# Performance work log

Measured on AMD Instinct MI355X. Metric: run time of the kernel, lower is better.

The kernel has to match this reference:

```python
import jax, jax.numpy as jnp
import numpy as np

N_NODES = 100000
N_EDGES = 1600000
DIMS = [128, 128, 128, 64]  # in, h1, h2, out


def setup_inputs() -> dict:
    key = jax.random.key(0)
    ks = jax.random.split(key, 12)
    inp = {
        "x": jax.random.normal(ks[0], (N_NODES, DIMS[0]), dtype=jnp.float32),
        "edge_index": jax.random.randint(ks[1], (2, N_EDGES), 0, N_NODES, dtype=jnp.int64),
        "edge_weights": jax.random.uniform(ks[2], (N_EDGES,), dtype=jnp.float32),
    }
    for i in range(3):
        inp[f"W{i+1}"] = jax.random.normal(ks[3 + 2 * i], (DIMS[i], DIMS[i + 1]), dtype=jnp.float32) * 0.05
        inp[f"b{i+1}"] = jax.random.normal(ks[4 + 2 * i], (DIMS[i + 1],), dtype=jnp.float32) * 0.01
    return inp


def gcn_conv(x, src, dst, w, W, b, n_nodes):
    # PyG GCNConv: linear transform, symmetric gcn_norm with self-loops (weight 1), scatter-add, bias.
    xw = x @ W                                            # [N, out]
    deg = jax.ops.segment_sum(w, dst, num_segments=n_nodes) + 1.0  # self-loop weight 1
    dinv = jnp.where(deg > 0, jax.lax.rsqrt(deg), 0.0)    # deg^{-1/2}
    norm = dinv[src] * w * dinv[dst]                      # [E]
    out = jax.ops.segment_sum(norm[:, None] * xw[src], dst, num_segments=n_nodes)
    out = out + (dinv * dinv)[:, None] * xw               # self-loop message
    return out + b


def reference(x, edge_index, edge_weights, W1, b1, W2, b2, W3, b3):
    src, dst = edge_index[0], edge_index[1]
    n = x.shape[0]
    # layer 1: GCNConv -> dropout(p=0) -> relu
    h = jax.nn.relu(gcn_conv(x, src, dst, edge_weights, W1, b1, n))
    # layer 2
    h = jax.nn.relu(gcn_conv(h, src, dst, edge_weights, W2, b2, n))
    # layer 3: activation 'none' -> Identity
    h = gcn_conv(h, src, dst, edge_weights, W3, b3, n)
    return h
```

## Files before the change

kernel.cpp:

```cpp
#include <hip/hip_runtime.h>
#include <hip/hip_fp16.h>
#include <math.h>


typedef __bf16 bf16x8 __attribute__((ext_vector_type(8)));
typedef float f32x4 __attribute__((ext_vector_type(4)));

union BF8 {
  unsigned short u[8];
  uint4 q;
  bf16x8 v;
};

__device__ __forceinline__ unsigned short rne_bf16(float f) {
  unsigned u = __float_as_uint(f);
  u += 0x7fff + ((u >> 16) & 1);
  return (unsigned short)(u >> 16);
}
__device__ __forceinline__ float bf16_to_f(unsigned short h) {
  return __uint_as_float((unsigned)h << 16);
}

__global__ __launch_bounds__(256) void prep_w1_kernel(const float* __restrict__ W,
    unsigned short* __restrict__ WTg) {
  const int t = threadIdx.x;
#pragma unroll
  for (int it = 0; it < 8; ++it) {
    int n = t % 128;
    int kc = it * 2 + t / 128;
    int k0 = kc * 8;
    BF8 hh, ll;
#pragma unroll
    for (int j = 0; j < 8; ++j) {
      float w = W[(size_t)(k0 + j) * 128 + n];
      unsigned short hb = rne_bf16(w);
      hh.u[j] = hb;
      ll.u[j] = rne_bf16(w - bf16_to_f(hb));
    }
    int kk = k0 ^ ((n & 7) << 3);
    *(uint4*)&WTg[(size_t)n * 128 + kk] = hh.q;
    *(uint4*)&WTg[16384 + (size_t)n * 128 + kk] = ll.q;
  }
}

__device__ __forceinline__ void gemm_body_g(const float* __restrict__ A,
    const unsigned short* __restrict__ WTg, unsigned short* __restrict__ Ch,
    int M, int bid) {
  constexpr int NF = 8;
  const int t = threadIdx.x;
  const int wv = t >> 6;
  const int l = t & 63;
  const int lr = l & 15;
  const int lg = l >> 4;
  const int arow_i = bid * 64 + wv * 16 + lr;
  const bool rv = arow_i < M;
  const float* arow = A + (size_t)arow_i * 128;

  f32x4 acc[NF] = {};
  float4 p0 = make_float4(0.f, 0.f, 0.f, 0.f), p1 = p0;
  if (rv) {
    p0 = *(const float4*)&arow[lg * 8];
    p1 = *(const float4*)&arow[lg * 8 + 4];
  }
#pragma unroll 1
  for (int ks = 0; ks < 4; ++ks) {
    int nkb = ((ks < 3) ? (ks + 1) * 32 : ks * 32) + lg * 8;
    float4 q0 = make_float4(0.f, 0.f, 0.f, 0.f), q1 = q0;
    if (rv) {
      q0 = *(const float4*)&arow[nkb];
      q1 = *(const float4*)&arow[nkb + 4];
    }
    float av[8] = {p0.x, p0.y, p0.z, p0.w, p1.x, p1.y, p1.z, p1.w};
    BF8 ah, al;
#pragma unroll
    for (int j = 0; j < 8; ++j) {
      unsigned short hb = rne_bf16(av[j]);
      ah.u[j] = hb;
      al.u[j] = rne_bf16(av[j] - bf16_to_f(hb));
    }
    int kidx = ks * 32 + lg * 8;
#pragma unroll
    for (int nf = 0; nf < NF; ++nf) {
      int n = nf * 16 + lr;
      int kk = kidx ^ ((n & 7) << 3);
      BF8 bh, bl;
      bh.q = *(const uint4*)&WTg[(size_t)n * 128 + kk];
      bl.q = *(const uint4*)&WTg[16384 + (size_t)n * 128 + kk];
      acc[nf] = __builtin_amdgcn_mfma_f32_16x16x32_bf16(ah.v, bh.v, acc[nf], 0, 0, 0);
      acc[nf] = __builtin_amdgcn_mfma_f32_16x16x32_bf16(al.v, bh.v, acc[nf], 0, 0, 0);
      acc[nf] = __builtin_amdgcn_mfma_f32_16x16x32_bf16(ah.v, bl.v, acc[nf], 0, 0, 0);
    }
    p0 = q0; p1 = q1;
  }
  const int orow0 = bid * 64 + wv * 16 + lg * 4;
#pragma unroll
  for (int j = 0; j < 4; ++j) {
    int orow = orow0 + j;
    if (orow < M) {
      unsigned short* hr = Ch + (size_t)orow * 128;
#pragma unroll
      for (int nf = 0; nf < NF; ++nf)
        hr[nf * 16 + lr] = __half_as_ushort(__float2half(acc[nf][j]));
    }
  }
}

__global__ __launch_bounds__(256) void pre_gemm_fused_kernel(
    const float* __restrict__ x, const unsigned short* __restrict__ WT1g,
    unsigned short* __restrict__ Ch, int M,
    const int* __restrict__ ei, const float* __restrict__ ew,
    unsigned long long* __restrict__ packed, int* __restrict__ rank,
    int E, int edgeBlocks) {
  if ((int)blockIdx.x < edgeBlocks) {
    int e = blockIdx.x * 256 + threadIdx.x;
    if (e >= E) return;
    int d = ei[E + e];
    unsigned wfix = (unsigned)__float2uint_rn(ew[e] * 16777216.0f);
    unsigned long long inc = (1ULL << 32) | (unsigned long long)wfix;
    unsigned long long old = atomicAdd(&packed[d], inc);
    rank[e] = (int)(old >> 32);
  } else {
    gemm_body_g(x, WT1g, Ch, M, blockIdx.x - edgeBlocks);
  }
}

template <int NCOL>
__global__ __launch_bounds__(256) void gemm_mfma_kernel(
    const unsigned short* __restrict__ Ah, const float* __restrict__ W,
    unsigned short* __restrict__ Ch, int M) {
  constexpr int NF = NCOL / 16;
  __shared__ __align__(16) unsigned short WT[2][NCOL][128];
  const int t = threadIdx.x;
  constexpr int KC_PER_IT = 256 / NCOL;
#pragma unroll
  for (int it = 0; it < 16 / KC_PER_IT; ++it) {
    int n = t % NCOL;
    int kc = it * KC_PER_IT + t / NCOL;
    int k0 = kc * 8;
    BF8 hh, ll;
#pragma unroll
    for (int j = 0; j < 8; ++j) {
      float w = W[(size_t)(k0 + j) * NCOL + n];
      unsigned short hb = rne_bf16(w);
      hh.u[j] = hb;
      ll.u[j] = rne_bf16(w - bf16_to_f(hb));
    }
    int kk = k0 ^ ((n & 7) << 3);
    *(uint4*)&WT[0][n][kk] = hh.q;
    *(uint4*)&WT[1][n][kk] = ll.q;
  }
  __syncthreads();

  const int wv = t >> 6;
  const int l = t & 63;
  const int lr = l & 15;
  const int lg = l >> 4;
  const int arow_i = blockIdx.x * 64 + wv * 16 + lr;
  const bool rv = arow_i < M;
  const unsigned short* arowh = Ah + (size_t)arow_i * 128;

  f32x4 acc[NF] = {};
  uint4 ph = make_uint4(0, 0, 0, 0);
  if (rv) ph = *(const uint4*)&arowh[lg * 8];
#pragma unroll 1
  for (int ks = 0; ks < 4; ++ks) {
    int nkb = ((ks < 3) ? (ks + 1) * 32 : ks * 32) + lg * 8;
    uint4 qh = make_uint4(0, 0, 0, 0);
    if (rv) qh = *(const uint4*)&arowh[nkb];
    float av[8];
    {
      union { uint4 q; __half2 h2[4]; } uu;
      uu.q = ph;
#pragma unroll
      for (int j = 0; j < 4; ++j) {
        float2 f = __half22float2(uu.h2[j]);
        av[j * 2] = f.x; av[j * 2 + 1] = f.y;
      }
    }
    BF8 ah, al;
#pragma unroll
    for (int j = 0; j < 8; ++j) {
      unsigned short hb = rne_bf16(av[j]);
      ah.u[j] = hb;
      al.u[j] = rne_bf16(av[j] - bf16_to_f(hb));
    }
    int kidx = ks * 32 + lg * 8;
    BF8 bh[NF], bl[NF];
#pragma unroll
    for (int nf = 0; nf < NF; ++nf) {
      int n = nf * 16 + lr;
      int kk = kidx ^ ((n & 7) << 3);
      bh[nf].q = *(const uint4*)&WT[0][n][kk];
      bl[nf].q = *(const uint4*)&WT[1][n][kk];
    }
#pragma unroll
    for (int nf = 0; nf < NF; ++nf) {
      acc[nf] = __builtin_amdgcn_mfma_f32_16x16x32_bf16(ah.v, bh[nf].v, acc[nf], 0, 0, 0);
      acc[nf] = __builtin_amdgcn_mfma_f32_16x16x32_bf16(al.v, bh[nf].v, acc[nf], 0, 0, 0);
      acc[nf] = __builtin_amdgcn_mfma_f32_16x16x32_bf16(ah.v, bl[nf].v, acc[nf], 0, 0, 0);
    }
    ph = qh;
  }
  const int orow0 = blockIdx.x * 64 + wv * 16 + lg * 4;
#pragma unroll
  for (int j = 0; j < 4; ++j) {
    int orow = orow0 + j;
    if (orow < M) {
      unsigned short* hr = Ch + (size_t)orow * NCOL;
#pragma unroll
      for (int nf = 0; nf < NF; ++nf)
        hr[nf * 16 + lr] = __half_as_ushort(__float2half(acc[nf][j]));
    }
  }
}

__global__ __launch_bounds__(256) void dinv_kernel(const unsigned long long* __restrict__ packed,
    float* __restrict__ dinv, int n) {
  int i = blockIdx.x * 256 + threadIdx.x;
  if (i >= n) return;
  float deg = 1.0f + (float)(unsigned)(packed[i] & 0xffffffffULL) * (1.0f / 16777216.0f);
  dinv[i] = 1.0f / sqrtf(deg);
}

__global__ __launch_bounds__(1024) void scanA(const unsigned long long* __restrict__ packed,
    int* __restrict__ row_ptr, int* __restrict__ partials, int n) {
  __shared__ int sd[1024];
  int t = threadIdx.x;
  int i = blockIdx.x * 1024 + t;
  int v = (i < n) ? (int)(packed[i] >> 32) : 0;
  sd[t] = v;
  __syncthreads();
  for (int off = 1; off < 1024; off <<= 1) {
    int u = (t >= off) ? sd[t - off] : 0;
    __syncthreads();
    sd[t] += u;
    __syncthreads();
  }
  int incl = sd[t];
  if (i < n) row_ptr[i] = incl - v;
  if (t == 1023) partials[blockIdx.x] = incl;
}

__global__ __launch_bounds__(128) void scanB(int* partials, int nb) {
  __shared__ int sd[128];
  int t = threadIdx.x;
  int v = (t < nb) ? partials[t] : 0;
  sd[t] = v;
  __syncthreads();
  for (int off = 1; off < 128; off <<= 1) {
    int u = (t >= off) ? sd[t - off] : 0;
    __syncthreads();
    sd[t] += u;
    __syncthreads();
  }
  int incl = sd[t];
  partials[t] = incl - v;
  if (t == nb - 1) partials[255] = incl;
}

__global__ __launch_bounds__(1024) void scanC(int* row_ptr, const int* __restrict__ partials, int n) {
  int i = blockIdx.x * 1024 + threadIdx.x;
  if (i < n) row_ptr[i] += partials[blockIdx.x];
  if (i == 0) row_ptr[n] = partials[255];
}

__global__ __launch_bounds__(256) void fill_kernel(const int* __restrict__ ei,
    const float* __restrict__ ew, const float* __restrict__ dinv,
    const int* __restrict__ row_ptr, const int* __restrict__ rank,
    int2* __restrict__ epair, int E) {
  int e = blockIdx.x * 256 + threadIdx.x;
  if (e >= E) return;
  int s = ei[e], d = ei[E + e];
  float nw = dinv[s] * ew[e] * dinv[d];
  int p = row_ptr[d] + rank[e];
  epair[p] = make_int2(s, __float_as_int(nw));
}

template <int F, bool RELU, bool OUTF16>
__global__ __launch_bounds__(256) void agg_kernel(const unsigned short* __restrict__ xwh,
    const int* __restrict__ row_ptr, const int2* __restrict__ epair,
    const float* __restrict__ dinv, const float* __restrict__ bias,
    void* __restrict__ out, int Nn) {
  constexpr int LPN = F / 4;
  int t = blockIdx.x * 256 + threadIdx.x;
  int node = t / LPN;
  int lane = t % LPN;
  if (node >= Nn) return;
  const uint2* xh = (const uint2*)xwh;
  int start = row_ptr[node];
  int end = row_ptr[node + 1];
  float a0x = 0.f, a0y = 0.f, a0z = 0.f, a0w = 0.f;
  float a1x = 0.f, a1y = 0.f, a1z = 0.f, a1w = 0.f;
  int p = start;
  for (; p + 4 <= end; p += 4) {
    int2 e0 = epair[p];
    int2 e1 = epair[p + 1];
    int2 e2 = epair[p + 2];
    int2 e3 = epair[p + 3];
    uint2 u0 = xh[(size_t)e0.x * LPN + lane];
    uint2 u1 = xh[(size_t)e1.x * LPN + lane];
    uint2 u2 = xh[(size_t)e2.x * LPN + lane];
    uint2 u3 = xh[(size_t)e3.x * LPN + lane];
    float n0 = __int_as_float(e0.y), n1 = __int_as_float(e1.y);
    float n2 = __int_as_float(e2.y), n3 = __int_as_float(e3.y);
    float2 f0a = __half22float2(*(__half2*)&u0.x), f0b = __half22float2(*(__half2*)&u0.y);
    float2 f1a = __half22float2(*(__half2*)&u1.x), f1b = __half22float2(*(__half2*)&u1.y);
    float2 f2a = __half22float2(*(__half2*)&u2.x), f2b = __half22float2(*(__half2*)&u2.y);
    float2 f3a = __half22float2(*(__half2*)&u3.x), f3b = __half22float2(*(__half2*)&u3.y);
    a0x = fmaf(n0, f0a.x, a0x); a0y = fmaf(n0, f0a.y, a0y);
    a0z = fmaf(n0, f0b.x, a0z); a0w = fmaf(n0, f0b.y, a0w);
    a1x = fmaf(n1, f1a.x, a1x); a1y = fmaf(n1, f1a.y, a1y);
    a1z = fmaf(n1, f1b.x, a1z); a1w = fmaf(n1, f1b.y, a1w);
    a0x = fmaf(n2, f2a.x, a0x); a0y = fmaf(n2, f2a.y, a0y);
    a0z = fmaf(n2, f2b.x, a0z); a0w = fmaf(n2, f2b.y, a0w);
    a1x = fmaf(n3, f3a.x, a1x); a1y = fmaf(n3, f3a.y, a1y);
    a1z = fmaf(n3, f3b.x, a1z); a1w = fmaf(n3, f3b.y, a1w);
  }
  for (; p < end; ++p) {
    int2 pr = epair[p];
    float nw = __int_as_float(pr.y);
    uint2 u = xh[(size_t)pr.x * LPN + lane];
    float2 fa = __half22float2(*(__half2*)&u.x), fb = __half22float2(*(__half2*)&u.y);
    a0x = fmaf(nw, fa.x, a0x); a0y = fmaf(nw, fa.y, a0y);
    a0z = fmaf(nw, fb.x, a0z); a0w = fmaf(nw, fb.y, a0w);
  }
  float di = dinv[node];
  float sw = di * di;
  uint2 su = xh[(size_t)node * LPN + lane];
  float2 sa = __half22float2(*(__half2*)&su.x), sb = __half22float2(*(__half2*)&su.y);
  a0x = fmaf(sw, sa.x, a0x); a0y = fmaf(sw, sa.y, a0y);
  a0z = fmaf(sw, sb.x, a0z); a0w = fmaf(sw, sb.y, a0w);
  float4 b = ((const float4*)bias)[lane];
  float ox = a0x + a1x + b.x;
  float oy = a0y + a1y + b.y;
  float oz = a0z + a1z + b.z;
  float ow = a0w + a1w + b.w;
  if (RELU) {
    ox = fmaxf(ox, 0.f); oy = fmaxf(oy, 0.f);
    oz = fmaxf(oz, 0.f); ow = fmaxf(ow, 0.f);
  }
  if constexpr (OUTF16) {
    uint2 o;
    __half2 h0 = __float22half2_rn(make_float2(ox, oy));
    __half2 h1 = __float22half2_rn(make_float2(oz, ow));
    o.x = *reinterpret_cast<unsigned*>(&h0);
    o.y = *reinterpret_cast<unsigned*>(&h1);
    ((uint2*)out)[(size_t)node * LPN + lane] = o;
  } else {
    ((float4*)out)[(size_t)node * LPN + lane] = make_float4(ox, oy, oz, ow);
  }
}

extern "C" void kernel_launch(void* const* d_in, const int* in_sizes, int n_in,
                              void* d_out, int out_size, void* d_ws, size_t ws_size,
                              hipStream_t stream) {
  const float* x  = (const float*)d_in[0];
  const int*   ei = (const int*)d_in[1];
  const float* ew = (const float*)d_in[2];
  const float* W1 = (const float*)d_in[3];
  const float* b1 = (const float*)d_in[4];
  const float* W2 = (const float*)d_in[5];
  const float* b2 = (const float*)d_in[6];
  const float* W3 = (const float*)d_in[7];
  const float* b3 = (const float*)d_in[8];

  const int N = in_sizes[0] / 128;
  const int E = in_sizes[2];

  char* ws = (char*)d_ws;
  size_t off = 0;
  auto carve = [&](size_t bytes) -> void* {
    void* p = ws + off;
    off += (bytes + 255) & ~(size_t)255;
    return p;
  };
  unsigned long long* packed = (unsigned long long*)carve((size_t)N * 8);
  int*   rank    = (int*)carve((size_t)E * 4);
  float* dinv    = (float*)carve((size_t)N * 4);
  int*   row_ptr = (int*)carve((size_t)(N + 1) * 4);
  int*   parts   = (int*)carve(256 * 4);
  int2*  epair   = (int2*)carve((size_t)E * 8);
  unsigned short* bufH = (unsigned short*)carve((size_t)N * 128 * 2);
  unsigned short* bufI = (unsigned short*)carve((size_t)N * 128 * 2);
  unsigned short* WT1g = (unsigned short*)carve(2 * 128 * 128 * 2);
  (void)ws_size; (void)n_in; (void)out_size;

  const int nThreads = 256;
  int gN  = (N + nThreads - 1) / nThreads;
  int gE  = (E + nThreads - 1) / nThreads;
  int nb  = (N + 1023) / 1024;
  const int gMM = (N + 63) / 64;
  int gAgg128 = (N * 32 + nThreads - 1) / nThreads;
  int gAgg64  = (N * 16 + nThreads - 1) / nThreads;

  hipMemsetAsync(packed, 0, (size_t)N * 8, stream);
  prep_w1_kernel<<<1, nThreads, 0, stream>>>(W1, WT1g);

  pre_gemm_fused_kernel<<<gE + gMM, nThreads, 0, stream>>>(
      x, WT1g, bufH, N, ei, ew, packed, rank, E, gE);

  dinv_kernel<<<gN, nThreads, 0, stream>>>(packed, dinv, N);
  scanA<<<nb, 1024, 0, stream>>>(packed, row_ptr, parts, N);
  scanB<<<1, 128, 0, stream>>>(parts, nb);
  scanC<<<nb, 1024, 0, stream>>>(row_ptr, parts, N);
  fill_kernel<<<gE, nThreads, 0, stream>>>(ei, ew, dinv, row_ptr, rank, epair, E);

  agg_kernel<128, true, true><<<gAgg128, nThreads, 0, stream>>>(bufH, row_ptr, epair, dinv, b1, bufI, N);

  gemm_mfma_kernel<128><<<gMM, nThreads, 0, stream>>>(bufI, W2, bufH, N);
  agg_kernel<128, true, true><<<gAgg128, nThreads, 0, stream>>>(bufH, row_ptr, epair, dinv, b2, bufI, N);

  gemm_mfma_kernel<64><<<gMM, nThreads, 0, stream>>>(bufI, W3, bufH, N);
  agg_kernel<64, false, false><<<gAgg64, nThreads, 0, stream>>>(bufH, row_ptr, epair, dinv, b3, d_out, N);
}
```

Baseline: 366.1 us.

## Split layer-1 GEMM into 64-column slices with per-block LDS weight staging

Removes the separate W1 prep kernel. Each GEMM block now converts a 64-column slice of W1 into hi/lo bf16 in shared memory and reads B fragments from LDS instead of global memory, with twice as many blocks each computing half the columns. Fragment loads are also batched ahead of the MFMA chain. The cost is that every block redoes the W1 split and reads its A rows twice across the column halves, and the shared-memory allocation may lower occupancy for the fused edge-atomic blocks.

```diff
diff --git a/kernel.cpp b/kernel.cpp
--- a/kernel.cpp
+++ b/kernel.cpp
@@ -21,33 +21,31 @@
   return __uint_as_float((unsigned)h << 16);
 }
 
-__global__ __launch_bounds__(256) void prep_w1_kernel(const float* __restrict__ W,
-    unsigned short* __restrict__ WTg) {
+__device__ __forceinline__ void gemm_body_slice(const float* __restrict__ A,
+    const float* __restrict__ W, int ldw, int col0,
+    unsigned short* __restrict__ Ch, int ldc, int M, int bid) {
+  constexpr int NF = 4;
+  __shared__ __align__(16) unsigned short WT[2][64][128];
   const int t = threadIdx.x;
 #pragma unroll
-  for (int it = 0; it < 8; ++it) {
-    int n = t % 128;
-    int kc = it * 2 + t / 128;
+  for (int it = 0; it < 4; ++it) {
+    int n = t & 63;
+    int kc = it * 4 + (t >> 6);
     int k0 = kc * 8;
     BF8 hh, ll;
 #pragma unroll
     for (int j = 0; j < 8; ++j) {
-      float w = W[(size_t)(k0 + j) * 128 + n];
+      float w = W[(size_t)(k0 + j) * ldw + col0 + n];
       unsigned short hb = rne_bf16(w);
       hh.u[j] = hb;
       ll.u[j] = rne_bf16(w - bf16_to_f(hb));
     }
     int kk = k0 ^ ((n & 7) << 3);
-    *(uint4*)&WTg[(size_t)n * 128 + kk] = hh.q;
-    *(uint4*)&WTg[16384 + (size_t)n * 128 + kk] = ll.q;
-  }
-}
-
-__device__ __forceinline__ void gemm_body_g(const float* __restrict__ A,
-    const unsigned short* __restrict__ WTg, unsigned short* __restrict__ Ch,
-    int M, int bid) {
-  constexpr int NF = 8;
-  const int t = threadIdx.x;
+    *(uint4*)&WT[0][n][kk] = hh.q;
+    *(uint4*)&WT[1][n][kk] = ll.q;
+  }
+  __syncthreads();
+
   const int wv = t >> 6;
   const int l = t & 63;
   const int lr = l & 15;
@@ -79,16 +77,19 @@
       al.u[j] = rne_bf16(av[j] - bf16_to_f(hb));
     }
     int kidx = ks * 32 + lg * 8;
+    BF8 bh[NF], bl[NF];
 #pragma unroll
     for (int nf = 0; nf < NF; ++nf) {
       int n = nf * 16 + lr;
       int kk = kidx ^ ((n & 7) << 3);
-      BF8 bh, bl;
-      bh.q = *(const uint4*)&WTg[(size_t)n * 128 + kk];
-      bl.q = *(const uint4*)&WTg[16384 + (size_t)n * 128 + kk];
-      acc[nf] = __builtin_amdgcn_mfma_f32_16x16x32_bf16(ah.v, bh.v, acc[nf], 0, 0, 0);
-      acc[nf] = __builtin_amdgcn_mfma_f32_16x16x32_bf16(al.v, bh.v, acc[nf], 0, 0, 0);
-      acc[nf] = __builtin_amdgcn_mfma_f32_16x16x32_bf16(ah.v, bl.v, acc[nf], 0, 0, 0);
+      bh[nf].q = *(const uint4*)&WT[0][n][kk];
+      bl[nf].q = *(const uint4*)&WT[1][n][kk];
+    }
+#pragma unroll
+    for (int nf = 0; nf < NF; ++nf) {
+      acc[nf] = __builtin_amdgcn_mfma_f32_16x16x32_bf16(ah.v, bh[nf].v, acc[nf], 0, 0, 0);
+      acc[nf] = __builtin_amdgcn_mfma_f32_16x16x32_bf16(al.v, bh[nf].v, acc[nf], 0, 0, 0);
+      acc[nf] = __builtin_amdgcn_mfma_f32_16x16x32_bf16(ah.v, bl[nf].v, acc[nf], 0, 0, 0);
     }
     p0 = q0; p1 = q1;
   }
@@ -97,7 +98,7 @@
   for (int j = 0; j < 4; ++j) {
     int orow = orow0 + j;
     if (orow < M) {
-      unsigned short* hr = Ch + (size_t)orow * 128;
+      unsigned short* hr = Ch + (size_t)orow * ldc + col0;
 #pragma unroll
       for (int nf = 0; nf < NF; ++nf)
         hr[nf * 16 + lr] = __half_as_ushort(__float2half(acc[nf][j]));
@@ -106,7 +107,7 @@
 }
 
 __global__ __launch_bounds__(256) void pre_gemm_fused_kernel(
-    const float* __restrict__ x, const unsigned short* __restrict__ WT1g,
+    const float* __restrict__ x, const float* __restrict__ W1,
     unsigned short* __restrict__ Ch, int M,
     const int* __restrict__ ei, const float* __restrict__ ew,
     unsigned long long* __restrict__ packed, int* __restrict__ rank,
@@ -120,7 +121,8 @@
     unsigned long long old = atomicAdd(&packed[d], inc);
     rank[e] = (int)(old >> 32);
   } else {
-    gemm_body_g(x, WT1g, Ch, M, blockIdx.x - edgeBlocks);
+    int g = blockIdx.x - edgeBlocks;
+    gemm_body_slice(x, W1, 128, (g & 1) * 64, Ch, 128, M, g >> 1);
   }
 }
 
@@ -382,7 +384,6 @@
   int2*  epair   = (int2*)carve((size_t)E * 8);
   unsigned short* bufH = (unsigned short*)carve((size_t)N * 128 * 2);
   unsigned short* bufI = (unsigned short*)carve((size_t)N * 128 * 2);
-  unsigned short* WT1g = (unsigned short*)carve(2 * 128 * 128 * 2);
   (void)ws_size; (void)n_in; (void)out_size;
 
   const int nThreads = 256;
@@ -394,10 +395,8 @@
   int gAgg64  = (N * 16 + nThreads - 1) / nThreads;
 
   hipMemsetAsync(packed, 0, (size_t)N * 8, stream);
-  prep_w1_kernel<<<1, nThreads, 0, stream>>>(W1, WT1g);
-
-  pre_gemm_fused_kernel<<<gE + gMM, nThreads, 0, stream>>>(
-      x, WT1g, bufH, N, ei, ew, packed, rank, E, gE);
+  pre_gemm_fused_kernel<<<gE + 2 * gMM, nThreads, 0, stream>>>(
+      x, W1, bufH, N, ei, ew, packed, rank, E, gE);
 
   dinv_kernel<<<gN, nThreads, 0, stream>>>(packed, dinv, N);
   scanA<<<nb, 1024, 0, stream>>>(packed, row_ptr, parts, N);
```

Result: faster. 352.1 us (-3.8%).
